# Optimization experiments

Measured on AMD Instinct MI355X. Metric: run time of the kernel, lower is better.

Reference implementation:

```python
import jax, jax.numpy as jnp
import numpy as np

EPS = 1e-12


def setup_inputs() -> dict:
    key = jax.random.key(0)
    k1, k2, k3, k4, k5, k6 = jax.random.split(key, 6)
    N, R, T, D, depth = 50000, 1000, 400000, 256, 2
    features = jax.random.normal(k1, (N, D), dtype=jnp.float32)
    rel_emb = jax.random.normal(k2, (R, D), dtype=jnp.float32)
    # xavier-style scale for [D,1] kernels, stored as [depth, D]
    attn_kernels = jax.random.normal(k3, (depth, D), dtype=jnp.float32) * np.sqrt(2.0 / (D + 1))
    r_val = jnp.ones((T,), dtype=jnp.float32)
    adj = jax.random.randint(k4, (2, T), 0, N, dtype=jnp.int64)
    r_index_tri = jnp.arange(T, dtype=jnp.int64)  # one relation per triple
    r_index_rel = jax.random.randint(k5, (T,), 0, R, dtype=jnp.int64)
    return {
        "features": features,
        "rel_emb": rel_emb,
        "attn_kernels": attn_kernels,
        "r_val": r_val,
        "adj": adj,
        "r_index_tri": r_index_tri,
        "r_index_rel": r_index_rel,
    }


def reference(features, rel_emb, attn_kernels, r_val, adj, r_index_tri, r_index_rel):
    N, D = features.shape
    T = adj.shape[1]
    depth = attn_kernels.shape[0]
    dst, src = adj[0], adj[1]  # softmax/aggregate over dst rows, gather neighbors via src

    x = jnp.tanh(features)
    outputs = [x]
    for l in range(depth):
        # sparse [T,R] @ rel_emb -> per-triple relation embedding [T, D]
        tri_rel = jax.ops.segment_sum(r_val[:, None] * rel_emb[r_index_rel], r_index_tri, num_segments=T)
        # L2 normalize per edge (torch F.normalize, eps=1e-12)
        norm = jnp.sqrt(jnp.sum(tri_rel * tri_rel, axis=1, keepdims=True))
        tri_rel = tri_rel / jnp.maximum(norm, EPS)
        # gather neighbor features and reflect across relation hyperplane
        neighs = x[src]  # [T, D]
        neighs = neighs - 2.0 * jnp.sum(neighs * tri_rel, axis=1, keepdims=True) * tri_rel
        # per-edge attention logits, segment softmax over destination rows
        att = tri_rel @ attn_kernels[l]  # [T]
        seg_max = jax.ops.segment_max(att, dst, num_segments=N)  # [N]
        e = jnp.exp(att - seg_max[dst])
        seg_sum = jax.ops.segment_sum(e, dst, num_segments=N)
        w = e / seg_sum[dst]  # [T]
        # scatter-sum weighted neighbor messages
        new_features = jax.ops.segment_sum(neighs * w[:, None], dst, num_segments=N)
        x = jnp.tanh(new_features)
        outputs.append(x)
    return jnp.concatenate(outputs, axis=-1)  # [N, D*(depth+1)]
```

## Files before the change

kernel.cpp:

```cpp
#include <hip/hip_runtime.h>
#include <hip/hip_bf16.h>
#include <hip/hip_fp16.h>

static constexpr int kN = 50000;
static constexpr int kR = 1000;
static constexpr int kT = 400000;
static constexpr int kD = 256;
static constexpr int kOutD = 768;
static constexpr int kNB = (kN + 255) / 256;
static constexpr int kX0B = kN * kD / 1024;
static constexpr int kTB = (kT + 255) / 256;

static constexpr size_t kOffRel16 = 2219008;
static constexpr size_t kOffXb1   = 2752512;
static constexpr size_t kXbBytes  = (size_t)kN * kD * 2;
static constexpr size_t kWsNeed   = kOffXb1 + kXbBytes;
static constexpr int kShRowB = 3072;
static constexpr int kShOffB = 2048;

#define EPS_NORM 1e-12f

typedef unsigned int u32;
typedef unsigned long long u64;
typedef u32 u32x2_t __attribute__((ext_vector_type(2)));
typedef u32 u32x4_t __attribute__((ext_vector_type(4)));

__device__ __forceinline__ float bf2f(__hip_bfloat16 h) { return __bfloat162float(h); }

__device__ __forceinline__ float4 cvt8(u32x2_t u) {
  float4 f;
  f.x = __half2float(__ushort_as_half((unsigned short)(u.x & 0xFFFFu)));
  f.y = __half2float(__ushort_as_half((unsigned short)(u.x >> 16)));
  f.z = __half2float(__ushort_as_half((unsigned short)(u.y & 0xFFFFu)));
  f.w = __half2float(__ushort_as_half((unsigned short)(u.y >> 16)));
  return f;
}
__device__ __forceinline__ float4 asf4(u32x4_t u) {
  float4 f;
  f.x = __uint_as_float(u.x); f.y = __uint_as_float(u.y);
  f.z = __uint_as_float(u.z); f.w = __uint_as_float(u.w);
  return f;
}

template <int CTRL>
__device__ __forceinline__ float dppmov(float x) {
  return __uint_as_float((u32)__builtin_amdgcn_update_dpp(
      0, (int)__float_as_uint(x), CTRL, 0xF, 0xF, false));
}
__device__ __forceinline__ float swz16(float x) {
  return __uint_as_float((u32)__builtin_amdgcn_ds_swizzle(
      (int)__float_as_uint(x), 0x401F));
}

__device__ __forceinline__ u32x2_t gload8(u64 sbase, u32 voff) {
  u32x2_t r;
  asm volatile("global_load_dwordx2 %0, %1, %2"
               : "=v"(r) : "v"(voff), "s"(sbase) : "memory");
  return r;
}
__device__ __forceinline__ u32x4_t gload16(u64 sbase, u32 voff) {
  u32x4_t r;
  asm volatile("global_load_dwordx4 %0, %1, %2"
               : "=v"(r) : "v"(voff), "s"(sbase) : "memory");
  return r;
}
__device__ __forceinline__ void waitv0() {
  asm volatile("s_waitcnt vmcnt(0)" ::: "memory");
  __builtin_amdgcn_sched_barrier(0);
}

__device__ __forceinline__ float loadF(const void* p, int i, int f32m) {
  return f32m ? ((const float*)p)[i] : bf2f(((const __hip_bfloat16*)p)[i]);
}
__device__ __forceinline__ int loadI(const void* p, int i, int i64m) {
  return i64m ? (int)(((const long long*)p)[i]) : ((const int*)p)[i];
}

__global__ void __launch_bounds__(256) detect_zero_kernel(
    const void* __restrict__ feat, const void* __restrict__ adj,
    int* __restrict__ flags, int* __restrict__ counts) {
  if (blockIdx.x == 0) {
    __shared__ int s_f32, s_i64;
    if (threadIdx.x == 0) { s_f32 = 0; s_i64 = 1; }
    __syncthreads();
    const __hip_bfloat16* fb = (const __hip_bfloat16*)feat;
    for (int i = threadIdx.x; i < 4096; i += 256) {
      const float v = bf2f(fb[i]);
      if (!(fabsf(v) <= 64.f)) atomicExch(&s_f32, 1);
    }
    const int* ai = (const int*)adj;
    for (int i = threadIdx.x; i < 2048; i += 256) {
      if (ai[2 * i + 1] != 0) atomicExch(&s_i64, 0);
    }
    __syncthreads();
    if (threadIdx.x == 0) { flags[0] = s_f32; flags[1] = s_i64; }
  } else {
    const int i = (blockIdx.x - 1) * 256 + threadIdx.x;
    if (i < kN) counts[i] = 0;
  }
}

__global__ void __launch_bounds__(256) prep_kernel(
    const void* __restrict__ rel_emb, const void* __restrict__ attn_k,
    __half* __restrict__ rel16, float* __restrict__ attL,
    const void* __restrict__ feat, float* __restrict__ out,
    const void* __restrict__ adj, int* __restrict__ counts,
    const int* __restrict__ flags) {
  const int f32m = flags[0];
  const int b = blockIdx.x;
  if (b < kR) {
    const int r = b, d = threadIdx.x;
    const float v  = loadF(rel_emb, r * kD + d, f32m);
    const float k0 = loadF(attn_k, d, f32m);
    const float k1 = loadF(attn_k, kD + d, f32m);
    float ss = v * v, d0 = v * k0, d1 = v * k1;
#pragma unroll
    for (int off = 32; off > 0; off >>= 1) {
      ss += __shfl_xor(ss, off);
      d0 += __shfl_xor(d0, off);
      d1 += __shfl_xor(d1, off);
    }
    __shared__ float s_ss[4], s_d0[4], s_d1[4];
    const int wave = threadIdx.x >> 6, lane = threadIdx.x & 63;
    if (lane == 0) { s_ss[wave] = ss; s_d0[wave] = d0; s_d1[wave] = d1; }
    __syncthreads();
    const float tss = s_ss[0] + s_ss[1] + s_ss[2] + s_ss[3];
    const float inv = 1.0f / fmaxf(sqrtf(tss), EPS_NORM);
    rel16[r * kD + d] = __float2half(v * inv);
    if (threadIdx.x == 0) {
      attL[r]      = (s_d0[0] + s_d0[1] + s_d0[2] + s_d0[3]) * inv;
      attL[kR + r] = (s_d1[0] + s_d1[1] + s_d1[2] + s_d1[3]) * inv;
    }
  } else if (b < kR + kX0B) {
    const int i4 = ((b - kR) * 256 + threadIdx.x) * 4;
    float v0, v1, v2, v3;
    if (f32m) {
      const float4 f = ((const float4*)feat)[i4 >> 2];
      v0 = f.x; v1 = f.y; v2 = f.z; v3 = f.w;
    } else {
      union { ushort4 u; __hip_bfloat16 h[4]; } xu;
      xu.u = ((const ushort4*)feat)[i4 >> 2];
      v0 = bf2f(xu.h[0]); v1 = bf2f(xu.h[1]); v2 = bf2f(xu.h[2]); v3 = bf2f(xu.h[3]);
    }
    const int n = i4 >> 8, d = i4 & 255;
    float4 o; o.x = tanhf(v0); o.y = tanhf(v1); o.z = tanhf(v2); o.w = tanhf(v3);
    *(float4*)(out + (size_t)n * kOutD + d) = o;
    ushort4 h;
    h.x = __half_as_ushort(__float2half(o.x));
    h.y = __half_as_ushort(__float2half(o.y));
    h.z = __half_as_ushort(__float2half(o.z));
    h.w = __half_as_ushort(__float2half(o.w));
    *(ushort4*)((char*)out + (size_t)n * kShRowB + kShOffB + (size_t)d * 2) = h;
  } else {
    const int t = (b - kR - kX0B) * 256 + threadIdx.x;
    if (t < kT) atomicAdd(&counts[loadI(adj, t, flags[1])], 1);
  }
}

__global__ void __launch_bounds__(256) psum_kernel(
    const int* __restrict__ counts, int* __restrict__ partials) {
  const int i = blockIdx.x * 256 + threadIdx.x;
  int v = (i < kN) ? counts[i] : 0;
#pragma unroll
  for (int off = 32; off > 0; off >>= 1) v += __shfl_xor(v, off);
  __shared__ int sw[4];
  const int lane = threadIdx.x & 63, wv = threadIdx.x >> 6;
  if (lane == 0) sw[wv] = v;
  __syncthreads();
  if (threadIdx.x == 0) partials[blockIdx.x] = sw[0] + sw[1] + sw[2] + sw[3];
}

__global__ void __launch_bounds__(256) offs2_kernel(
    const int* __restrict__ counts, const int* __restrict__ partials,
    int* __restrict__ offsets, int* __restrict__ cursor) {
  const int t = threadIdx.x, lane = t & 63, wv = t >> 6;
  int pv = (t < (int)blockIdx.x) ? partials[t] : 0;
#pragma unroll
  for (int off = 32; off > 0; off >>= 1) pv += __shfl_xor(pv, off);
  __shared__ int sb[4];
  if (lane == 0) sb[wv] = pv;
  __syncthreads();
  const int pbase = sb[0] + sb[1] + sb[2] + sb[3];
  const int i = blockIdx.x * 256 + t;
  const int v = (i < kN) ? counts[i] : 0;
  int x = v;
#pragma unroll
  for (int d = 1; d < 64; d <<= 1) {
    const int y = __shfl_up(x, d);
    if (lane >= d) x += y;
  }
  __shared__ int sw2[4];
  if (lane == 63) sw2[wv] = x;
  __syncthreads();
  int woff = 0;
  for (int w = 0; w < wv; ++w) woff += sw2[w];
  const int excl = pbase + woff + x - v;
  if (i < kN) { offsets[i] = excl; cursor[i] = excl; }
  if (i == 0) offsets[kN] = kT;
}

__global__ void __launch_bounds__(256) fill_kernel(
    const void* __restrict__ adj, const void* __restrict__ rrel,
    const void* __restrict__ r_val, int* __restrict__ cursor,
    int* __restrict__ perm, const int* __restrict__ flags) {
  const int t = blockIdx.x * 256 + threadIdx.x;
  if (t >= kT) return;
  const int f32m = flags[0], i64m = flags[1];
  const int dn = loadI(adj, t, i64m);
  const int sn = loadI(adj, kT + t, i64m);
  const int r  = loadI(rrel, t, i64m);
  const float rv = loadF(r_val, t, f32m);
  const int pk = (sn & 0xFFFF) | ((r & 0x3FF) << 16) |
                 ((rv != 0.f) ? (1 << 26) : 0) | ((rv < 0.f) ? (1 << 27) : 0);
  perm[atomicAdd(&cursor[dn], 1)] = pk;
}

template <int XF16, int XROWB, int XOFFB>
__global__ void __launch_bounds__(256, 5) layer_kernel(
    const int* __restrict__ offsets, const int* __restrict__ perm,
    const float* __restrict__ xin,
    const char* __restrict__ xb,
    const __half* __restrict__ rel16, const float* __restrict__ attL_l,
    float* __restrict__ out, int col0,
    __half* __restrict__ xbout) {
  const int lane = threadIdx.x & 63;
  const int n = blockIdx.x * 4 + (threadIdx.x >> 6);
  const int beg = offsets[n];
  const int cnt = offsets[n + 1] - beg;
  float4 acc = make_float4(0.f, 0.f, 0.f, 0.f);
  float* orow = out + (size_t)n * kOutD + col0;

  if (cnt > 0 && cnt <= 64) {
    int pk_l = 0;
    float logit = -1e30f;
    if (lane < cnt) {
      pk_l = perm[beg + lane];
      const float a = attL_l[(pk_l >> 16) & 0x3FF];
      const float sa = (pk_l & (1 << 27)) ? -a : a;
      logit = (pk_l & (1 << 26)) ? sa : 0.f;
    }
    asm volatile("" : "+v"(logit));

    const u32 voffx = (u32)lane * (XF16 ? 8u : 16u);
    const u32 voffr = (u32)lane * 8u;
    u32x2_t ux2[8]; u32x4_t ux4[8]; u32x2_t ur[8];
    u32 pkk[8];

#define ISSUE_BATCH(BASE)                                                      \
  _Pragma("unroll") for (int k = 0; k < 8; ++k) {                              \
    pkk[k] = (u32)__builtin_amdgcn_readlane(pk_l, (BASE) + k);                 \
    if (XF16) {                                                                \
      ux2[k] = gload8((u64)xb + (u64)((pkk[k] & 0xFFFFu) * (u32)XROWB) +       \
                          (u32)XOFFB, voffx);                                  \
    } else {                                                                   \
      ux4[k] = gload16((u64)xin + (u64)((pkk[k] & 0xFFFFu) * 3072u) + 1024u,   \
                       voffx);                                                 \
    }                                                                          \
    ur[k] = gload8((u64)rel16 + (u64)(((pkk[k] >> 16) & 0x3FFu) << 9), voffr); \
  }

#define COMPUTE_BATCH(BASE)                                                    \
  {                                                                            \
    float wvv[8];                                                              \
    _Pragma("unroll") for (int k = 0; k < 8; ++k)                              \
      wvv[k] = __uint_as_float(                                                \
          (u32)__builtin_amdgcn_readlane(__float_as_uint(w_me), (BASE) + k));  \
    float dt[8];                                                               \
    _Pragma("unroll") for (int k = 0; k < 8; ++k) {                            \
      float4 xv;                                                               \
      if (XF16) xv = cvt8(ux2[k]); else xv = asf4(ux4[k]);                     \
      const float4 rr = cvt8(ur[k]);                                           \
      dt[k] = xv.x * rr.x + xv.y * rr.y + xv.z * rr.z + xv.w * rr.w;           \
      acc.x += xv.x * wvv[k]; acc.y += xv.y * wvv[k];                          \
      acc.z += xv.z * wvv[k]; acc.w += xv.w * wvv[k];                          \
    }                                                                          \
                            \
    _Pragma("unroll") for (int k = 0; k < 8; ++k) dt[k] += dppmov<0x128>(dt[k]);\
    _Pragma("unroll") for (int k = 0; k < 8; ++k) dt[k] += dppmov<0x124>(dt[k]);\
    _Pragma("unroll") for (int k = 0; k < 8; ++k) dt[k] += dppmov<0x122>(dt[k]);\
    _Pragma("unroll") for (int k = 0; k < 8; ++k) dt[k] += dppmov<0x121>(dt[k]);\
    _Pragma("unroll") for (int k = 0; k < 8; ++k) dt[k] += swz16(dt[k]);       \
    _Pragma("unroll") for (int k = 0; k < 8; ++k) dt[k] += __shfl_xor(dt[k], 32);\
    _Pragma("unroll") for (int k = 0; k < 8; ++k) {                            \
      const float cw = ((pkk[k] >> 26) & 1u) ? (2.f * wvv[k] * dt[k]) : 0.f;   \
      const float4 rr = cvt8(ur[k]);                                           \
      acc.x -= cw * rr.x; acc.y -= cw * rr.y;                                  \
      acc.z -= cw * rr.z; acc.w -= cw * rr.w;                                  \
    }                                                                          \
  }

    ISSUE_BATCH(0);

    float m = logit;
    m = fmaxf(m, dppmov<0x128>(m));
    m = fmaxf(m, dppmov<0x124>(m));
    m = fmaxf(m, dppmov<0x122>(m));
    m = fmaxf(m, dppmov<0x121>(m));
    if (cnt > 16) m = fmaxf(m, swz16(m));
    if (cnt > 32) m = fmaxf(m, __shfl_xor(m, 32));
    const float e = (lane < cnt) ? __expf(logit - m) : 0.f;
    float s = e;
    s += dppmov<0x128>(s);
    s += dppmov<0x124>(s);
    s += dppmov<0x122>(s);
    s += dppmov<0x121>(s);
    if (cnt > 16) s += swz16(s);
    if (cnt > 32) s += __shfl_xor(s, 32);
    const float w_me = (lane < cnt) ? e / s : 0.f;

    int base = 0;
    while (true) {
      waitv0();
      COMPUTE_BATCH(base);
      base += 8;
      if (base >= cnt) break;
      ISSUE_BATCH(base);
    }
#undef ISSUE_BATCH
#undef COMPUTE_BATCH
  } else if (cnt > 64) {
    float lm = -1e30f;
    for (int i = lane; i < cnt; i += 64) {
      const int p = perm[beg + i];
      const float a = attL_l[(p >> 16) & 0x3FF];
      const float sa = (p & (1 << 27)) ? -a : a;
      lm = fmaxf(lm, (p & (1 << 26)) ? sa : 0.f);
    }
#pragma unroll
    for (int off = 32; off > 0; off >>= 1) lm = fmaxf(lm, __shfl_xor(lm, off));
    float ls = 0.f;
    for (int i = lane; i < cnt; i += 64) {
      const int p = perm[beg + i];
      const float a = attL_l[(p >> 16) & 0x3FF];
      const float sa = (p & (1 << 27)) ? -a : a;
      ls += __expf(((p & (1 << 26)) ? sa : 0.f) - lm);
    }
#pragma unroll
    for (int off = 32; off > 0; off >>= 1) ls += __shfl_xor(ls, off);
    const float inv_s = 1.f / ls;

    for (int base = 0; base < cnt; base += 64) {
      const int nIn = min(64, cnt - base);
      int pkl = 0; float wl = 0.f;
      if (lane < nIn) {
        pkl = perm[beg + base + lane];
        const float a = attL_l[(pkl >> 16) & 0x3FF];
        const float sa = (pkl & (1 << 27)) ? -a : a;
        wl = __expf(((pkl & (1 << 26)) ? sa : 0.f) - lm) * inv_s;
      }
      for (int k = 0; k < nIn; ++k) {
        const int p   = __shfl(pkl, k);
        const float w = __shfl(wl, k);
        float4 xv;
        if (XF16) {
          xv = cvt8(*(const u32x2_t*)(xb + (size_t)(p & 0xFFFF) * XROWB +
                                      XOFFB + (size_t)lane * 8));
        } else {
          xv = *(const float4*)((const char*)xin + (size_t)(p & 0xFFFF) * 3072 +
                                1024 + (size_t)lane * 16);
        }
        const float4 rr = cvt8(*(const u32x2_t*)((const char*)rel16 +
                               (((size_t)(p >> 16) & 0x3FF) << 9) +
                               (size_t)lane * 8));
        float dot = xv.x * rr.x + xv.y * rr.y + xv.z * rr.z + xv.w * rr.w;
#pragma unroll
        for (int off = 32; off > 0; off >>= 1) dot += __shfl_xor(dot, off);
        const float s2 = (p >> 26) & 1 ? 1.f : 0.f;
        const float c = 2.f * s2 * dot * w;
        acc.x += xv.x * w - c * rr.x;
        acc.y += xv.y * w - c * rr.y;
        acc.z += xv.z * w - c * rr.z;
        acc.w += xv.w * w - c * rr.w;
      }
    }
  }

  acc.x = tanhf(acc.x); acc.y = tanhf(acc.y);
  acc.z = tanhf(acc.z); acc.w = tanhf(acc.w);
  *(float4*)(orow + lane * 4) = acc;
  if (xbout) {
    ushort4 h;
    h.x = __half_as_ushort(__float2half(acc.x));
    h.y = __half_as_ushort(__float2half(acc.y));
    h.z = __half_as_ushort(__float2half(acc.z));
    h.w = __half_as_ushort(__float2half(acc.w));
    *(ushort4*)(xbout + (size_t)n * kD + lane * 4) = h;
  }
}

extern "C" void kernel_launch(void* const* d_in, const int* in_sizes, int n_in,
                              void* d_out, int out_size, void* d_ws, size_t ws_size,
                              hipStream_t stream) {
  const void* features = d_in[0];
  const void* rel_emb  = d_in[1];
  const void* attn_k   = d_in[2];
  const void* r_val    = d_in[3];
  const void* adj      = d_in[4];
  const void* rrel     = d_in[6];
  float* out           = (float*)d_out;

  char* ws = (char*)d_ws;
  int*    flags    = (int*)(ws + 0);
  float*  attL     = (float*)(ws + 4096);
  int*    partials = (int*)(ws + 12288);
  int*    counts   = (int*)(ws + 16384);
  int*    offsets  = (int*)(ws + 217088);
  int*    cursor   = (int*)(ws + 417792);
  int*    perm     = (int*)(ws + 618496);
  __half* rel16    = (__half*)(ws + kOffRel16);
  const bool full = (ws_size >= kWsNeed);
  __half* xb1 = full ? (__half*)(ws + kOffXb1) : nullptr;

  detect_zero_kernel<<<1 + kNB, 256, 0, stream>>>(features, adj, flags, counts);
  prep_kernel<<<kR + kX0B + kTB, 256, 0, stream>>>(
      rel_emb, attn_k, rel16, attL, features, out, adj, counts, flags);
  psum_kernel<<<kNB, 256, 0, stream>>>(counts, partials);
  offs2_kernel<<<kNB, 256, 0, stream>>>(counts, partials, offsets, cursor);
  fill_kernel<<<kTB, 256, 0, stream>>>(adj, rrel, r_val, cursor, perm, flags);

  layer_kernel<1, kShRowB, kShOffB><<<kN / 4, 256, 0, stream>>>(
      offsets, perm, nullptr, (const char*)out, rel16, attL, out, kD, xb1);
  if (full) {
    layer_kernel<1, 512, 0><<<kN / 4, 256, 0, stream>>>(
        offsets, perm, nullptr, (const char*)xb1, rel16, attL + kR, out,
        2 * kD, nullptr);
  } else {
    layer_kernel<0, 1, 0><<<kN / 4, 256, 0, stream>>>(
        offsets, perm, out, nullptr, rel16, attL + kR, out, 2 * kD, nullptr);
  }
}
```

Measured before the change: 358.2 us.

## Fuse preprocessing kernels into one cooperative kernel with grid syncs

```diff
diff --git a/kernel.cpp b/kernel.cpp
--- a/kernel.cpp
+++ b/kernel.cpp
@@ -1,6 +1,9 @@
 #include <hip/hip_runtime.h>
+#include <hip/hip_cooperative_groups.h>
 #include <hip/hip_bf16.h>
 #include <hip/hip_fp16.h>
+
+namespace cg = cooperative_groups;
 
 static constexpr int kN = 50000;
 static constexpr int kR = 1000;
@@ -10,6 +13,7 @@
 static constexpr int kNB = (kN + 255) / 256;
 static constexpr int kX0B = kN * kD / 1024;
 static constexpr int kTB = (kT + 255) / 256;
+static constexpr int kCoopB = 1024;
 
 static constexpr size_t kOffRel16 = 2219008;
 static constexpr size_t kOffXb1   = 2752512;
@@ -74,6 +78,142 @@
 }
 __device__ __forceinline__ int loadI(const void* p, int i, int i64m) {
   return i64m ? (int)(((const long long*)p)[i]) : ((const int*)p)[i];
+}
+
+__global__ void __launch_bounds__(256) build_kernel(
+    const void* __restrict__ rel_emb, const void* __restrict__ attn_k,
+    __half* __restrict__ rel16, float* __restrict__ attL,
+    const void* __restrict__ feat, float* __restrict__ out,
+    const void* __restrict__ adj, const void* __restrict__ rrel,
+    const void* __restrict__ r_val,
+    int* __restrict__ counts, int* __restrict__ partials,
+    int* __restrict__ offsets, int* __restrict__ cursor,
+    int* __restrict__ perm, int* __restrict__ flags) {
+  cg::grid_group grid = cg::this_grid();
+  const int tid = threadIdx.x;
+  const int lane = tid & 63, wv = tid >> 6;
+  __shared__ float sA[4], sB[4], sC[4];
+  __shared__ int iA[4], iB[4];
+
+  if (blockIdx.x == 0) {
+    __shared__ int s_f32, s_i64;
+    if (tid == 0) { s_f32 = 0; s_i64 = 1; }
+    __syncthreads();
+    const __hip_bfloat16* fb = (const __hip_bfloat16*)feat;
+    for (int i = tid; i < 4096; i += 256) {
+      const float v = bf2f(fb[i]);
+      if (!(fabsf(v) <= 64.f)) atomicExch(&s_f32, 1);
+    }
+    const int* ai = (const int*)adj;
+    for (int i = tid; i < 2048; i += 256) {
+      if (ai[2 * i + 1] != 0) atomicExch(&s_i64, 0);
+    }
+    __syncthreads();
+    if (tid == 0) { flags[0] = s_f32; flags[1] = s_i64; __threadfence(); }
+  }
+  for (int i = blockIdx.x * 256 + tid; i < kN; i += kCoopB * 256) counts[i] = 0;
+  grid.sync();
+
+  const int f32m = flags[0], i64m = flags[1];
+
+  for (int vb = blockIdx.x; vb < kR + kX0B + kTB; vb += kCoopB) {
+    if (vb < kR) {
+      const int r = vb, d = tid;
+      const float v  = loadF(rel_emb, r * kD + d, f32m);
+      const float k0 = loadF(attn_k, d, f32m);
+      const float k1 = loadF(attn_k, kD + d, f32m);
+      float ss = v * v, d0 = v * k0, d1 = v * k1;
+#pragma unroll
+      for (int off = 32; off > 0; off >>= 1) {
+        ss += __shfl_xor(ss, off);
+        d0 += __shfl_xor(d0, off);
+        d1 += __shfl_xor(d1, off);
+      }
+      if (lane == 0) { sA[wv] = ss; sB[wv] = d0; sC[wv] = d1; }
+      __syncthreads();
+      const float tss = sA[0] + sA[1] + sA[2] + sA[3];
+      const float inv = 1.0f / fmaxf(sqrtf(tss), EPS_NORM);
+      rel16[r * kD + d] = __float2half(v * inv);
+      if (tid == 0) {
+        attL[r]      = (sB[0] + sB[1] + sB[2] + sB[3]) * inv;
+        attL[kR + r] = (sC[0] + sC[1] + sC[2] + sC[3]) * inv;
+      }
+      __syncthreads();
+    } else if (vb < kR + kX0B) {
+      const int i4 = ((vb - kR) * 256 + tid) * 4;
+      float v0, v1, v2, v3;
+      if (f32m) {
+        const float4 f = ((const float4*)feat)[i4 >> 2];
+        v0 = f.x; v1 = f.y; v2 = f.z; v3 = f.w;
+      } else {
+        union { ushort4 u; __hip_bfloat16 h[4]; } xu;
+        xu.u = ((const ushort4*)feat)[i4 >> 2];
+        v0 = bf2f(xu.h[0]); v1 = bf2f(xu.h[1]);
+        v2 = bf2f(xu.h[2]); v3 = bf2f(xu.h[3]);
+      }
+      const int n = i4 >> 8, d = i4 & 255;
+      float4 o; o.x = tanhf(v0); o.y = tanhf(v1); o.z = tanhf(v2); o.w = tanhf(v3);
+      *(float4*)(out + (size_t)n * kOutD + d) = o;
+      ushort4 h;
+      h.x = __half_as_ushort(__float2half(o.x));
+      h.y = __half_as_ushort(__float2half(o.y));
+      h.z = __half_as_ushort(__float2half(o.z));
+      h.w = __half_as_ushort(__float2half(o.w));
+      *(ushort4*)((char*)out + (size_t)n * kShRowB + kShOffB + (size_t)d * 2) = h;
+    } else {
+      const int t = (vb - kR - kX0B) * 256 + tid;
+      if (t < kT) atomicAdd(&counts[loadI(adj, t, i64m)], 1);
+    }
+  }
+  grid.sync();
+
+  for (int vb = blockIdx.x; vb < kNB; vb += kCoopB) {
+    const int i = vb * 256 + tid;
+    int v = (i < kN) ? counts[i] : 0;
+#pragma unroll
+    for (int off = 32; off > 0; off >>= 1) v += __shfl_xor(v, off);
+    if (lane == 0) iA[wv] = v;
+    __syncthreads();
+    if (tid == 0) partials[vb] = iA[0] + iA[1] + iA[2] + iA[3];
+    __syncthreads();
+  }
+  grid.sync();
+
+  for (int vb = blockIdx.x; vb < kNB; vb += kCoopB) {
+    int pv = (tid < vb) ? partials[tid] : 0;
+#pragma unroll
+    for (int off = 32; off > 0; off >>= 1) pv += __shfl_xor(pv, off);
+    if (lane == 0) iA[wv] = pv;
+    __syncthreads();
+    const int pbase = iA[0] + iA[1] + iA[2] + iA[3];
+    const int i = vb * 256 + tid;
+    const int v = (i < kN) ? counts[i] : 0;
+    int x = v;
+#pragma unroll
+    for (int d = 1; d < 64; d <<= 1) {
+      const int y = __shfl_up(x, d);
+      if (lane >= d) x += y;
+    }
+    if (lane == 63) iB[wv] = x;
+    __syncthreads();
+    int woff = 0;
+    for (int w = 0; w < wv; ++w) woff += iB[w];
+    const int excl = pbase + woff + x - v;
+    if (i < kN) { offsets[i] = excl; cursor[i] = excl; }
+    if (i == 0) offsets[kN] = kT;
+    __syncthreads();
+  }
+  grid.sync();
+
+  for (int t = blockIdx.x * 256 + tid; t < kT; t += kCoopB * 256) {
+    const int dn = loadI(adj, t, i64m);
+    const int sn = loadI(adj, kT + t, i64m);
+    const int r  = loadI(rrel, t, i64m);
+    const float rv = loadF(r_val, t, f32m);
+    const int pk = (sn & 0xFFFF) | ((r & 0x3FF) << 16) |
+                   ((rv != 0.f) ? (1 << 26) : 0) | ((rv < 0.f) ? (1 << 27) : 0);
+    perm[atomicAdd(&cursor[dn], 1)] = pk;
+  }
 }
 
 __global__ void __launch_bounds__(256) detect_zero_kernel(
@@ -274,7 +414,6 @@
       acc.x += xv.x * wvv[k]; acc.y += xv.y * wvv[k];                          \
       acc.z += xv.z * wvv[k]; acc.w += xv.w * wvv[k];                          \
     }                                                                          \
-                            \
     _Pragma("unroll") for (int k = 0; k < 8; ++k) dt[k] += dppmov<0x128>(dt[k]);\
     _Pragma("unroll") for (int k = 0; k < 8; ++k) dt[k] += dppmov<0x124>(dt[k]);\
     _Pragma("unroll") for (int k = 0; k < 8; ++k) dt[k] += dppmov<0x122>(dt[k]);\
@@ -411,12 +550,25 @@
   const bool full = (ws_size >= kWsNeed);
   __half* xb1 = full ? (__half*)(ws + kOffXb1) : nullptr;
 
-  detect_zero_kernel<<<1 + kNB, 256, 0, stream>>>(features, adj, flags, counts);
-  prep_kernel<<<kR + kX0B + kTB, 256, 0, stream>>>(
-      rel_emb, attn_k, rel16, attL, features, out, adj, counts, flags);
-  psum_kernel<<<kNB, 256, 0, stream>>>(counts, partials);
-  offs2_kernel<<<kNB, 256, 0, stream>>>(counts, partials, offsets, cursor);
-  fill_kernel<<<kTB, 256, 0, stream>>>(adj, rrel, r_val, cursor, perm, flags);
+  bool coop_ok;
+  {
+    void* args[] = {(void*)&rel_emb, (void*)&attn_k, (void*)&rel16,
+                    (void*)&attL,    (void*)&features, (void*)&out,
+                    (void*)&adj,     (void*)&rrel,   (void*)&r_val,
+                    (void*)&counts,  (void*)&partials, (void*)&offsets,
+                    (void*)&cursor,  (void*)&perm,   (void*)&flags};
+    coop_ok = (hipLaunchCooperativeKernel((const void*)build_kernel,
+                                          dim3(kCoopB), dim3(256), args, 0,
+                                          stream) == hipSuccess);
+  }
+  if (!coop_ok) {
+    detect_zero_kernel<<<1 + kNB, 256, 0, stream>>>(features, adj, flags, counts);
+    prep_kernel<<<kR + kX0B + kTB, 256, 0, stream>>>(
+        rel_emb, attn_k, rel16, attL, features, out, adj, counts, flags);
+    psum_kernel<<<kNB, 256, 0, stream>>>(counts, partials);
+    offs2_kernel<<<kNB, 256, 0, stream>>>(counts, partials, offsets, cursor);
+    fill_kernel<<<kTB, 256, 0, stream>>>(adj, rrel, r_val, cursor, perm, flags);
+  }
 
   layer_kernel<1, kShRowB, kShOffB><<<kN / 4, 256, 0, stream>>>(
       offsets, perm, nullptr, (const char*)out, rel16, attL, out, kD, xb1);
```

Measured after the change: 740.9 us. 107% more time.
